# Optimization experiments

Hardware: AMD Instinct MI355X
Metric: run time of the kernel (lower is better)

## Reference

```python
import jax, jax.numpy as jnp
import numpy as np

B, S, V, E, H, C = 16384, 64, 25, 64, 64, 3

def setup_inputs() -> dict:
    key = jax.random.key(0)
    ks = jax.random.split(key, 5)
    return {
        "messages": jax.random.normal(ks[0], (B, S, V), dtype=jnp.float32),
        "embedding": jax.random.normal(ks[1], (V, E), dtype=jnp.float32) * 0.1,
        "W_ih": jax.random.normal(ks[2], (4 * H, E), dtype=jnp.float32) * 0.1,
        "W_hh": jax.random.normal(ks[3], (4 * H, H), dtype=jnp.float32) * 0.1,
        "b_ih": jnp.zeros((4 * H,), dtype=jnp.float32),
        "b_hh": jnp.zeros((4 * H,), dtype=jnp.float32).at[H:2 * H].set(1.0),
        "fc_w": jax.random.normal(ks[4], (C, H), dtype=jnp.float32) * 0.1,
        "fc_b": jnp.zeros((C,), dtype=jnp.float32),
    }

def _lstm_forward(emb_t, W_ih, W_hh, b_ih, b_hh):
    # emb_t: [S, B, E] time-major. PyTorch LSTMCell gate order: i, f, g, o.
    batch = emb_t.shape[1]
    h0 = jnp.zeros((batch, W_hh.shape[1]), dtype=emb_t.dtype)
    c0 = jnp.zeros_like(h0)
    # Precompute input projections for all steps in one big GEMM.
    x_proj = jnp.einsum('sbe,ge->sbg', emb_t, W_ih) + b_ih + b_hh  # [S, B, 4H]

    def step(carry, xp):
        h, c = carry
        gates = xp + h @ W_hh.T  # [B, 4H]
        i, f, g, o = jnp.split(gates, 4, axis=-1)
        i = jax.nn.sigmoid(i)
        f = jax.nn.sigmoid(f)
        g = jnp.tanh(g)
        o = jax.nn.sigmoid(o)
        c_new = f * c + i * g
        h_new = o * jnp.tanh(c_new)
        return (h_new, c_new), None

    (h_final, _), _ = jax.lax.scan(step, (h0, c0), x_proj)
    return h_final

def reference(messages, embedding, W_ih, W_hh, b_ih, b_hh, fc_w, fc_b):
    emb = jnp.einsum('bsv,ve->bse', messages, embedding)  # [B, S, E]
    emb_t = jnp.transpose(emb, (1, 0, 2))                 # [S, B, E]
    h = _lstm_forward(emb_t, W_ih, W_hh, b_ih, b_hh)      # [B, H]
    fc_out = h @ fc_w.T + fc_b                            # [B, C]
    return jnp.squeeze(fc_out)
```

## Files before the change

kernel.cpp:

```cpp
#include <hip/hip_runtime.h>
#include <math.h>


using bf16x8 = __attribute__((ext_vector_type(8))) short;
using f32x4  = __attribute__((ext_vector_type(4))) float;
using f32x2  = __attribute__((ext_vector_type(2))) float;

union U16B { uint4 u; bf16x8 v; };

#define KE  1.4426950408889634f
#define K2E 2.8853900817779268f

__device__ __forceinline__ unsigned short f2bf(float x) {
    unsigned int u = __float_as_uint(x);
    u += 0x7FFFu + ((u >> 16) & 1u);
    return (unsigned short)(u >> 16);
}
__device__ __forceinline__ float bf2f(unsigned short h) {
    return __uint_as_float(((unsigned int)h) << 16);
}

__global__ void prep_kernel(const float* __restrict__ emb,
                            const float* __restrict__ Wih,
                            const float* __restrict__ Whh,
                            const float* __restrict__ bih,
                            const float* __restrict__ bhh,
                            unsigned short* __restrict__ wfrag) {
    const int b = blockIdx.x, tid = threadIdx.x;
    const int ch = b >> 4, gt = b & 15;
    const int lane = tid >> 3, j = tid & 7;
    const int kloc = (lane >> 4) * 8 + j;
    const int gunit = 16 * gt + (lane & 15);
    float v = 0.f;
    if (ch == 0) {
        if (kloc < 25) {
            const float* ep = emb + kloc * 64;
            const float* wp = Wih + gunit * 64;
            float s = 0.f;
            #pragma unroll
            for (int e = 0; e < 64; ++e) s = fmaf(ep[e], wp[e], s);
            v = s;
        } else if (kloc == 25) {
            v = bih[gunit] + bhh[gunit];
        }
    } else {
        v = Whh[gunit * 64 + (ch - 1) * 32 + kloc];
    }
    const int gate = gunit >> 6;
    const float s = (gate == 2) ? K2E : -KE;
    wfrag[((ch * 16 + gt) * 64 + lane) * 8 + j] = f2bf(s * v);
}

#define CVTPK(D, A, B_)                                                      \
    asm("v_cvt_pk_bf16_f32 %0, %1, %2" : "=v"(D) : "v"(A), "v"(B_));

#define BARRIER()                                                            \
    asm volatile("s_waitcnt lgkmcnt(0)\n\ts_barrier" ::: "memory");

#define LOADMSG(DST, PTR)                                                    \
    {                                                                        \
        const float* p_ = (PTR) + kq;                                        \
        if (kq < 24) {                                                       \
            _Pragma("unroll") for (int j = 0; j < 8; ++j) DST[j] = p_[j];    \
        } else {                                                             \
            DST[0] = p_[0]; DST[1] = 1.0f;                \
            _Pragma("unroll") for (int j = 2; j < 8; ++j) DST[j] = 0.f;      \
        }                                                                    \
    }

#define CONVMSG(MB, MF)                                                      \
    {                                                                        \
        CVTPK(MB.u.x, MF[0], MF[1]) CVTPK(MB.u.y, MF[2], MF[3])              \
        CVTPK(MB.u.z, MF[4], MF[5]) CVTPK(MB.u.w, MF[6], MF[7])              \
    }

#define STEP(S, CURB, NXTB, MF)                                              \
    {                                                                        \
        bf16x8 bh0, bh1;                                                     \
        {                                                                    \
            int o0_ = (l16 * 128 + 0 * 64 + lq * 16) ^ swz;                  \
            int o1_ = (l16 * 128 + 1 * 64 + lq * 16) ^ swz;                  \
            bh0 = *(const bf16x8*)((CURB) + o0_);                            \
            bh1 = *(const bf16x8*)((CURB) + o1_);                            \
        }                                                                    \
        U16B mc_;                                                            \
        CONVMSG(mc_, MF)                                                     \
        if ((S) < 62) { LOADMSG(MF, mp) }                                    \
        mp += 25;                                                            \
        f32x4 acc[4];                                                        \
        _Pragma("unroll") for (int i = 0; i < 4; ++i)                        \
            acc[i] = __builtin_amdgcn_mfma_f32_16x16x32_bf16(                \
                w[0][i], mc_.v, z4, 0, 0, 0);                                \
        _Pragma("unroll") for (int i = 0; i < 4; ++i)                        \
            acc[i] = __builtin_amdgcn_mfma_f32_16x16x32_bf16(                \
                w[1][i], bh0, acc[i], 0, 0, 0);                              \
        _Pragma("unroll") for (int i = 0; i < 4; ++i)                        \
            acc[i] = __builtin_amdgcn_mfma_f32_16x16x32_bf16(                \
                w[2][i], bh1, acc[i], 0, 0, 0);                              \
        unsigned hw0_, hw1_;                                                 \
        _Pragma("unroll") for (int pp = 0; pp < 2; ++pp) {                   \
            f32x2 ai, af, ag, ao;                                            \
            ai[0] = acc[0][2*pp]; ai[1] = acc[0][2*pp+1];                    \
            af[0] = acc[1][2*pp]; af[1] = acc[1][2*pp+1];                    \
            ag[0] = acc[2][2*pp]; ag[1] = acc[2][2*pp+1];                    \
            ao[0] = acc[3][2*pp]; ao[1] = acc[3][2*pp+1];                    \
            f32x2 ti, tf_, tg, to_;                                          \
            ti[0]  = __builtin_amdgcn_exp2f(ai[0]);                          \
            ti[1]  = __builtin_amdgcn_exp2f(ai[1]);                          \
            tf_[0] = __builtin_amdgcn_exp2f(af[0]);                          \
            tf_[1] = __builtin_amdgcn_exp2f(af[1]);                          \
            to_[0] = __builtin_amdgcn_exp2f(ao[0]);                          \
            to_[1] = __builtin_amdgcn_exp2f(ao[1]);                          \
            tg[0]  = __builtin_amdgcn_exp2f(-fabsf(ag[0]));                  \
            tg[1]  = __builtin_amdgcn_exp2f(-fabsf(ag[1]));                  \
            f32x2 F_ = tf_ + 1.f;                                            \
            f32x2 P_ = (ti + 1.f) * (tg + 1.f);                              \
            f32x2 D_ = P_ * F_;                                              \
            f32x2 G_ = (1.f - tg) * F_;                                      \
            G_[0] = copysignf(G_[0], ag[0]);                                 \
            G_[1] = copysignf(G_[1], ag[1]);                                 \
            f32x2 num_ = c2[pp] * P_ + G_;                                   \
            f32x2 rD_;                                                       \
            rD_[0] = __builtin_amdgcn_rcpf(D_[0]);                           \
            rD_[1] = __builtin_amdgcn_rcpf(D_[1]);                           \
            f32x2 cn_ = num_ * rD_;                                          \
            c2[pp] = cn_;                                                    \
            f32x2 kc_ = cn_ * K2E;                                           \
            f32x2 tc_;                                                       \
            tc_[0] = __builtin_amdgcn_exp2f(-fabsf(kc_[0]));                 \
            tc_[1] = __builtin_amdgcn_exp2f(-fabsf(kc_[1]));                 \
            f32x2 D2_ = (to_ + 1.f) * (tc_ + 1.f);                           \
            f32x2 rD2_;                                                      \
            rD2_[0] = __builtin_amdgcn_rcpf(D2_[0]);                         \
            rD2_[1] = __builtin_amdgcn_rcpf(D2_[1]);                         \
            f32x2 ot_ = (1.f - tc_) * rD2_;                                  \
            float h0_ = copysignf(ot_[0], cn_[0]);                           \
            float h1_ = copysignf(ot_[1], cn_[1]);                           \
            if (pp == 0) { CVTPK(hw0_, h0_, h1_) }                           \
            else         { CVTPK(hw1_, h0_, h1_) }                           \
        }                                                                    \
        *(uint2*)((NXTB) + offw) = make_uint2(hw0_, hw1_);                   \
        BARRIER()                                                            \
    }

__global__ __launch_bounds__(256, 4) void lstm_mfma(
    const float* __restrict__ msgs,
    const unsigned short* __restrict__ wfrag,
    const float* __restrict__ fcw,
    const float* __restrict__ fcb,
    float* __restrict__ out)
{
    __shared__ __align__(16) char lds[4096];

    const int tid  = threadIdx.x;
    const int lane = tid & 63;
    const int cg   = __builtin_amdgcn_readfirstlane(tid >> 6);
    const int l16  = lane & 15;
    const int lq   = lane >> 4;
    const int row0 = blockIdx.x * 16;
    const int kq   = lq * 8;

    bf16x8 w[3][4];
    #pragma unroll
    for (int ch = 0; ch < 3; ++ch)
        #pragma unroll
        for (int i = 0; i < 4; ++i)
            w[ch][i] = *(const bf16x8*)(wfrag + ((ch * 16 + 4 * i + cg) * 64 + lane) * 8);

    for (int idx = tid; idx < 512; idx += 256) ((unsigned int*)lds)[idx] = 0u;

    const f32x4 z4 = (f32x4){0.f, 0.f, 0.f, 0.f};

    f32x2 c2[2];
    c2[0] = (f32x2){0.f, 0.f};
    c2[1] = (f32x2){0.f, 0.f};

    const float* mrow = msgs + (long)(row0 + l16) * 1600;
    const float* mp   = mrow + 50;
    const int swz  = (l16 & 7) << 4;
    const int offw = (l16 * 128 + cg * 32 + lq * 8) ^ swz;

    float mfA[8], mfB[8];
    LOADMSG(mfA, mrow)
    LOADMSG(mfB, mrow + 25)
    __syncthreads();

    char* b0 = (char*)lds;
    char* b1 = b0 + 2048;
    for (int s2 = 0; s2 < 64; s2 += 2) {
        STEP(s2,     b0, b1, mfA)
        STEP(s2 + 1, b1, b0, mfB)
    }

    if (tid < 64) {
        const int r = tid >> 2, cls = tid & 3;
        if (cls < 3) {
            float a = fcb[cls];
            const int sw = (r & 7) << 4;
            #pragma unroll
            for (int u = 0; u < 64; ++u) {
                int off = (r * 128 + u * 2) ^ sw;
                float hv = bf2f(*(const unsigned short*)(b0 + off));
                a = fmaf(hv, fcw[cls * 64 + u], a);
            }
            out[(row0 + r) * 3 + cls] = a;
        }
    }
}

extern "C" void kernel_launch(void* const* d_in, const int* in_sizes, int n_in,
                              void* d_out, int out_size, void* d_ws, size_t ws_size,
                              hipStream_t stream) {
    const float* msgs = (const float*)d_in[0];
    const float* emb  = (const float*)d_in[1];
    const float* Wih  = (const float*)d_in[2];
    const float* Whh  = (const float*)d_in[3];
    const float* bih  = (const float*)d_in[4];
    const float* bhh  = (const float*)d_in[5];
    const float* fcw  = (const float*)d_in[6];
    const float* fcb  = (const float*)d_in[7];
    float* out = (float*)d_out;

    unsigned short* wfrag = (unsigned short*)d_ws;

    prep_kernel<<<48, 512, 0, stream>>>(emb, Wih, Whh, bih, bhh, wfrag);
    lstm_mfma<<<16384 / 16, 256, 0, stream>>>(msgs, wfrag, fcw, fcb, out);
}
```

Measured before the change: 92.47 us.

## Interleave two independent 16-row LSTM tiles per block to hide recurrence latency

Each block now handles 32 batch rows as two independent 16-row tiles. Each tile has its own LDS double buffer, cell state and message pointer. The two tiles' steps are interleaved so that one barrier covers both, which gives the scheduler independent MFMA and transcendental work to overlap within the serial recurrence. In exchange, register pressure roughly doubles (launch bounds drop from 4 to 2 blocks per CU), LDS per block doubles, and the grid is halved.

```diff
diff --git a/kernel.cpp b/kernel.cpp
--- a/kernel.cpp
+++ b/kernel.cpp
@@ -74,19 +74,15 @@
         CVTPK(MB.u.z, MF[4], MF[5]) CVTPK(MB.u.w, MF[6], MF[7])              \
     }
 
-#define STEP(S, CURB, NXTB, MF)                                              \
+#define STEP(S, CURB, NXTB, MF, C2, OFFW, MP)                                \
     {                                                                        \
         bf16x8 bh0, bh1;                                                     \
-        {                                                                    \
-            int o0_ = (l16 * 128 + 0 * 64 + lq * 16) ^ swz;                  \
-            int o1_ = (l16 * 128 + 1 * 64 + lq * 16) ^ swz;                  \
-            bh0 = *(const bf16x8*)((CURB) + o0_);                            \
-            bh1 = *(const bf16x8*)((CURB) + o1_);                            \
-        }                                                                    \
+        bh0 = *(const bf16x8*)((CURB) + ro0);                                \
+        bh1 = *(const bf16x8*)((CURB) + ro1);                                \
         U16B mc_;                                                            \
         CONVMSG(mc_, MF)                                                     \
-        if ((S) < 62) { LOADMSG(MF, mp) }                                    \
-        mp += 25;                                                            \
+        if ((S) < 62) { LOADMSG(MF, MP) }                                    \
+        MP += 25;                                                            \
         f32x4 acc[4];                                                        \
         _Pragma("unroll") for (int i = 0; i < 4; ++i)                        \
             acc[i] = __builtin_amdgcn_mfma_f32_16x16x32_bf16(                \
@@ -119,12 +115,12 @@
             f32x2 G_ = (1.f - tg) * F_;                                      \
             G_[0] = copysignf(G_[0], ag[0]);                                 \
             G_[1] = copysignf(G_[1], ag[1]);                                 \
-            f32x2 num_ = c2[pp] * P_ + G_;                                   \
+            f32x2 num_ = C2[pp] * P_ + G_;                                   \
             f32x2 rD_;                                                       \
             rD_[0] = __builtin_amdgcn_rcpf(D_[0]);                           \
             rD_[1] = __builtin_amdgcn_rcpf(D_[1]);                           \
             f32x2 cn_ = num_ * rD_;                                          \
-            c2[pp] = cn_;                                                    \
+            C2[pp] = cn_;                                                    \
             f32x2 kc_ = cn_ * K2E;                                           \
             f32x2 tc_;                                                       \
             tc_[0] = __builtin_amdgcn_exp2f(-fabsf(kc_[0]));                 \
@@ -139,25 +135,24 @@
             if (pp == 0) { CVTPK(hw0_, h0_, h1_) }                           \
             else         { CVTPK(hw1_, h0_, h1_) }                           \
         }                                                                    \
-        *(uint2*)((NXTB) + offw) = make_uint2(hw0_, hw1_);                   \
-        BARRIER()                                                            \
-    }
-
-__global__ __launch_bounds__(256, 4) void lstm_mfma(
+        *(uint2*)((NXTB) + (OFFW)) = make_uint2(hw0_, hw1_);                 \
+    }
+
+__global__ __launch_bounds__(256, 2) void lstm_mfma(
     const float* __restrict__ msgs,
     const unsigned short* __restrict__ wfrag,
     const float* __restrict__ fcw,
     const float* __restrict__ fcb,
     float* __restrict__ out)
 {
-    __shared__ __align__(16) char lds[4096];
+    __shared__ __align__(16) char lds[8192];
 
     const int tid  = threadIdx.x;
     const int lane = tid & 63;
     const int cg   = __builtin_amdgcn_readfirstlane(tid >> 6);
     const int l16  = lane & 15;
     const int lq   = lane >> 4;
-    const int row0 = blockIdx.x * 16;
+    const int row0 = blockIdx.x * 32;
     const int kq   = lq * 8;
 
     bf16x8 w[3][4];
@@ -167,40 +162,60 @@
         for (int i = 0; i < 4; ++i)
             w[ch][i] = *(const bf16x8*)(wfrag + ((ch * 16 + 4 * i + cg) * 64 + lane) * 8);
 
-    for (int idx = tid; idx < 512; idx += 256) ((unsigned int*)lds)[idx] = 0u;
+    for (int idx = tid; idx < 512; idx += 256) {
+        ((unsigned int*)lds)[idx] = 0u;
+        ((unsigned int*)(lds + 4096))[idx] = 0u;
+    }
 
     const f32x4 z4 = (f32x4){0.f, 0.f, 0.f, 0.f};
 
-    f32x2 c2[2];
-    c2[0] = (f32x2){0.f, 0.f};
-    c2[1] = (f32x2){0.f, 0.f};
-
-    const float* mrow = msgs + (long)(row0 + l16) * 1600;
-    const float* mp   = mrow + 50;
+    f32x2 c2a[2], c2b[2];
+    c2a[0] = (f32x2){0.f, 0.f}; c2a[1] = (f32x2){0.f, 0.f};
+    c2b[0] = (f32x2){0.f, 0.f}; c2b[1] = (f32x2){0.f, 0.f};
+
     const int swz  = (l16 & 7) << 4;
+    const int ro0  = (l16 * 128 + lq * 16) ^ swz;
+    const int ro1  = (l16 * 128 + 64 + lq * 16) ^ swz;
     const int offw = (l16 * 128 + cg * 32 + lq * 8) ^ swz;
 
-    float mfA[8], mfB[8];
-    LOADMSG(mfA, mrow)
-    LOADMSG(mfB, mrow + 25)
+    const float* mrow0 = msgs + (long)(row0 + l16) * 1600;
+    const float* mrow1 = msgs + (long)(row0 + 16 + l16) * 1600;
+
+    float mA0[8], mB0[8], mA1[8], mB1[8];
+    LOADMSG(mA0, mrow0)
+    LOADMSG(mB0, mrow0 + 25)
+    LOADMSG(mA1, mrow1)
+    LOADMSG(mB1, mrow1 + 25)
+    const float* mp0 = mrow0 + 50;
+    const float* mp1 = mrow1 + 50;
+
     __syncthreads();
 
-    char* b0 = (char*)lds;
-    char* b1 = b0 + 2048;
+    char* t0b0 = (char*)lds;
+    char* t0b1 = t0b0 + 2048;
+    char* t1b0 = t0b0 + 4096;
+    char* t1b1 = t0b0 + 6144;
+
     for (int s2 = 0; s2 < 64; s2 += 2) {
-        STEP(s2,     b0, b1, mfA)
-        STEP(s2 + 1, b1, b0, mfB)
-    }
-
-    if (tid < 64) {
+        STEP(s2, t0b0, t0b1, mA0, c2a, offw, mp0)
+        STEP(s2, t1b0, t1b1, mA1, c2b, offw, mp1)
+        BARRIER()
+        STEP(s2 + 1, t0b1, t0b0, mB0, c2a, offw, mp0)
+        STEP(s2 + 1, t1b1, t1b0, mB1, c2b, offw, mp1)
+        BARRIER()
+    }
+
+    if (tid < 128) {
         const int r = tid >> 2, cls = tid & 3;
         if (cls < 3) {
+            const char* hb = (r < 16) ? t0b0 : t1b0;
+            const int rr = r & 15;
             float a = fcb[cls];
-            const int sw = (r & 7) << 4;
+            const int sw = (rr & 7) << 4;
             #pragma unroll
             for (int u = 0; u < 64; ++u) {
-                int off = (r * 128 + u * 2) ^ sw;
-                float hv = bf2f(*(const unsigned short*)(b0 + off));
+                int off = (rr * 128 + u * 2) ^ sw;
+                float hv = bf2f(*(const unsigned short*)(hb + off));
                 a = fmaf(hv, fcw[cls * 64 + u], a);
             }
             out[(row0 + r) * 3 + cls] = a;
@@ -224,5 +239,5 @@
     unsigned short* wfrag = (unsigned short*)d_ws;
 
     prep_kernel<<<48, 512, 0, stream>>>(emb, Wih, Whh, bih, bhh, wfrag);
-    lstm_mfma<<<16384 / 16, 256, 0, stream>>>(msgs, wfrag, fcw, fcb, out);
-}
+    lstm_mfma<<<16384 / 32, 256, 0, stream>>>(msgs, wfrag, fcw, fcb, out);
+}
```

New measurement: 101.8 us. 10.1% more time.
